# Kernel optimization log

Measured on AMD Instinct MI355X. Metric: run time of the kernel, lower is better.

## Reference

```python
import jax, jax.numpy as jnp
import numpy as np
from jax import lax

EXP = 5      # exponent bits of the custom float format
MAN = 10     # mantissa bits
STRIDE = 1
PADDING = 1


def float_quantize(x, exp=EXP, man=MAN):
    """Round-to-nearest-even quantization to a custom (exp, man) float format,
    with exponent clamping to the subnormal range and saturation at max value.
    Uses a straight-through estimator so the op is differentiable."""
    emax = 2 ** (exp - 1) - 1
    emin = 1 - emax
    _, e = jnp.frexp(x)                      # x = m * 2^e, m in [0.5, 1)
    e = jnp.maximum(e - 1, emin)             # unbiased exponent, clamp to emin (subnormals)
    scale = jnp.exp2((e - man).astype(x.dtype))
    q = jnp.round(x / scale) * scale         # round half to even on the mantissa grid
    maxval = jnp.asarray((2.0 - 2.0 ** (-man)) * 2.0 ** emax, x.dtype)
    q = jnp.clip(q, -maxval, maxval)
    return x + lax.stop_gradient(q - x)      # straight-through


def quant_gemm(a, b):
    """a: [M, K], b: [K, N]. FMA-style GEMM where the product and the running
    accumulator are re-quantized to the (EXP, MAN) format at every k step,
    mimicking the custom low-precision accumulation loop."""
    M = a.shape[0]
    N = b.shape[1]

    def step(acc, ab):
        ak, bk = ab                          # ak: [M], bk: [N]
        prod = float_quantize(ak[:, None] * bk[None, :])
        return float_quantize(acc + prod), None

    acc0 = jnp.zeros((M, N), a.dtype)
    acc, _ = lax.scan(step, acc0, (a.T, b))
    return acc


def _unfold(x, kh, kw, stride, padding):
    """im2col matching torch.nn.functional.unfold: returns [B, OH*OW, C*kh*kw]."""
    B, C, H, W = x.shape
    oh = (H - kh + 2 * padding) // stride + 1
    ow = (W - kw + 2 * padding) // stride + 1
    xp = jnp.pad(x, ((0, 0), (0, 0), (padding, padding), (padding, padding)))
    cols = []
    for i in range(kh):
        for j in range(kw):
            cols.append(xp[:, :, i:i + (oh - 1) * stride + 1:stride,
                              j:j + (ow - 1) * stride + 1:stride])
    col = jnp.stack(cols, axis=2)            # [B, C, kh*kw, oh, ow]
    col = col.reshape(B, C * kh * kw, oh * ow)
    return col.transpose(0, 2, 1), oh, ow    # [B, M, K]


def setup_inputs() -> dict:
    key = jax.random.key(0)
    kx, kw_, kb = jax.random.split(key, 3)
    x = jax.random.normal(kx, (16, 32, 56, 56), dtype=jnp.float32)
    # kaiming-uniform-ish scale: fan_in = 32*3*3 = 288
    weight = jax.random.normal(kw_, (64, 32, 3, 3), dtype=jnp.float32) * (1.0 / np.sqrt(288.0))
    bias = jax.random.normal(kb, (64,), dtype=jnp.float32) * (1.0 / np.sqrt(288.0))
    return {"x": x, "weight": weight, "bias": bias}


def reference(x, weight, bias):
    B, C, H, W = x.shape
    N, Cg, kh, kw = weight.shape
    qw = float_quantize(weight)              # quantize weights
    qb = float_quantize(bias)                # quantize bias
    a, oh, ow = _unfold(x, kh, kw, STRIDE, PADDING)   # [B, M, K]
    K = C * kh * kw
    a2 = a.reshape(B * oh * ow, K)
    b2 = qw.reshape(N, K).T                  # [K, N]
    out = quant_gemm(a2, b2)                 # [B*M, N], low-precision accumulation
    out = out + qb[None, :]
    out = float_quantize(out)                # re-quantize output
    out = out.reshape(B, oh * ow, N).transpose(0, 2, 1)
    return out.reshape(B, N, oh, ow)
```

## Files before the change

### kernel.cpp

```cpp
#include <hip/hip_runtime.h>
#include <stdint.h>

typedef _Float16 f16x8 __attribute__((ext_vector_type(8)));
typedef float    f32x4 __attribute__((ext_vector_type(4)));

#define H 56
#define W 56
#define C_IN 32
#define N_OUT 64
#define PR 58
#define PCOLS 66
#define XB_BLOCKS (16 * PR)
#define NWF 9216
#define XPAD_BYTES ((size_t)16 * PR * PCOLS * C_IN * 2)

__device__ __forceinline__ float q16f(float v) { return (float)(_Float16)v; }

__global__ __launch_bounds__(256) void prep_kernel(
    const float* __restrict__ x, const float* __restrict__ weight,
    _Float16* __restrict__ xpad, uint32_t* __restrict__ wf)
{
    const int nb  = blockIdx.x;
    const int tid = threadIdx.x;
    if (nb < XB_BLOCKS) {
        __shared__ _Float16 sT[PCOLS * 34];
        for (int i = tid; i < PCOLS * 17; i += 256) ((uint32_t*)sT)[i] = 0u;
        __syncthreads();
        const int b = nb / PR, row = nb % PR, ih = row - 1;
        if ((unsigned)ih < (unsigned)H) {
            #pragma unroll
            for (int k = 0; k < 7; ++k) {
                int idx = k * 256 + tid;
                int c = idx / W, iw = idx - c * W;
                sT[(iw + 1) * 34 + c] = (_Float16)x[((b * C_IN + c) * H + ih) * W + iw];
            }
        }
        __syncthreads();
        uint32_t* dst = (uint32_t*)(xpad + ((size_t)b * PR + row) * PCOLS * C_IN);
        for (int i = tid; i < PCOLS * 16; i += 256) {
            int col = i >> 4, cd = i & 15;
            dst[i] = ((const uint32_t*)sT)[col * 17 + cd];
        }
    } else {
        int o = (nb - XB_BLOCKS) * 256 + tid;
        int t2   = o & 3;
        int lane = (o >> 2) & 63;
        int u    = o >> 8;
        int nt   = u & 3, ij = u >> 2;
        int n    = nt * 16 + (lane & 15);
        int c0   = (lane >> 4) * 8 + 2 * t2;
        _Float16 lo = (_Float16)weight[n * 288 + c0 * 9 + ij];
        _Float16 hi = (_Float16)weight[n * 288 + (c0 + 1) * 9 + ij];
        wf[o] = (uint32_t)__builtin_bit_cast(uint16_t, lo) |
                ((uint32_t)__builtin_bit_cast(uint16_t, hi) << 16);
    }
}

__global__ __launch_bounds__(256, 2) void conv_mfma(
    const _Float16* __restrict__ xpad,
    const f16x8*    __restrict__ wf,
    const float*    __restrict__ bias,
    float* __restrict__ out)
{
    const int tid  = threadIdx.x;
    const int b    = blockIdx.z;
    const int oh   = blockIdx.y * 4 + (tid >> 6);
    const int bx   = blockIdx.x;
    const int ow0  = bx * 24;
    const int lane = tid & 63;
    const int quad = lane >> 4;
    const int px   = lane & 15;

    const _Float16* xb0 = xpad + (((size_t)b * PR + oh) * PCOLS + ow0 + px) * C_IN + quad * 8;
    const _Float16* xb1 = xb0 + 16 * C_IN;

    f32x4 acc[2][4] = {{{0,0,0,0},{0,0,0,0},{0,0,0,0},{0,0,0,0}},
                       {{0,0,0,0},{0,0,0,0},{0,0,0,0},{0,0,0,0}}};

    #pragma unroll
    for (int ij = 0; ij < 9; ++ij) {
        const int i = ij / 3, jj = ij - 3 * i;
        const int sh = (i * PCOLS + jj) * C_IN;
        f16x8 xf0 = *(const f16x8*)(xb0 + sh);
        f16x8 xf1 = *(const f16x8*)(xb1 + sh);
        #pragma unroll
        for (int nt = 0; nt < 4; ++nt) {
            f16x8 wv = wf[(ij * 4 + nt) * 64 + lane];
            acc[0][nt] = __builtin_amdgcn_mfma_f32_16x16x32_f16(wv, xf0, acc[0][nt], 0, 0, 0);
            acc[1][nt] = __builtin_amdgcn_mfma_f32_16x16x32_f16(wv, xf1, acc[1][nt], 0, 0, 0);
        }
    }

    #pragma unroll
    for (int xg = 0; xg < 2; ++xg) {
        const int ow = ow0 + 16 * xg + px;
        if (bx == 0 || ow >= 32) {
            #pragma unroll
            for (int nt = 0; nt < 4; ++nt) {
                #pragma unroll
                for (int reg = 0; reg < 4; ++reg) {
                    const int n = nt * 16 + quad * 4 + reg;
                    out[((size_t)(b * N_OUT + n) * H + oh) * W + ow] =
                        q16f(acc[xg][nt][reg] + q16f(bias[n]));
                }
            }
        }
    }
}

extern "C" void kernel_launch(void* const* d_in, const int* in_sizes, int n_in,
                              void* d_out, int out_size, void* d_ws, size_t ws_size,
                              hipStream_t stream) {
    const float* x      = (const float*)d_in[0];
    const float* weight = (const float*)d_in[1];
    const float* bias   = (const float*)d_in[2];
    float* out          = (float*)d_out;

    _Float16* xpad = (_Float16*)d_ws;
    uint32_t* wfp  = (uint32_t*)((char*)d_ws + XPAD_BYTES);

    prep_kernel<<<dim3(XB_BLOCKS + NWF / 256), dim3(256), 0, stream>>>(x, weight, xpad, wfp);
    conv_mfma<<<dim3(2, 14, 16), dim3(256), 0, stream>>>(xpad, (const f16x8*)wfp, bias, out);
}
```

Baseline: 71.83 us.

## Fuse input padding/transposition and weight packing into the conv kernel via LDS

Removes the separate prep kernel that wrote a padded fp16 NHWC copy of the input and packed weight fragments to global memory. Each conv block now loads its input halo tile directly from the fp32 NCHW input into shared memory, padded to 40 channels per pixel, and repacks all weights into shared memory itself. This drops one launch and the global round trip for the intermediate tensor. In exchange, every block redundantly repacks the full weight set and reads the input with a strided gather, and the shared-memory footprint is larger.

```diff
diff --git a/kernel.cpp b/kernel.cpp
--- a/kernel.cpp
+++ b/kernel.cpp
@@ -8,84 +8,77 @@
 #define W 56
 #define C_IN 32
 #define N_OUT 64
-#define PR 58
-#define PCOLS 66
-#define XB_BLOCKS (16 * PR)
-#define NWF 9216
-#define XPAD_BYTES ((size_t)16 * PR * PCOLS * C_IN * 2)
+#define CP 40
 
 __device__ __forceinline__ float q16f(float v) { return (float)(_Float16)v; }
 
-__global__ __launch_bounds__(256) void prep_kernel(
-    const float* __restrict__ x, const float* __restrict__ weight,
-    _Float16* __restrict__ xpad, uint32_t* __restrict__ wf)
+__global__ __launch_bounds__(256, 3) void conv_fused(
+    const float* __restrict__ x,
+    const float* __restrict__ weight,
+    const float* __restrict__ bias,
+    float* __restrict__ out)
 {
-    const int nb  = blockIdx.x;
+    __shared__ __align__(16) uint32_t sW[9216];
+    __shared__ __align__(16) _Float16 sX[6 * 34 * CP];
+
     const int tid = threadIdx.x;
-    if (nb < XB_BLOCKS) {
-        __shared__ _Float16 sT[PCOLS * 34];
-        for (int i = tid; i < PCOLS * 17; i += 256) ((uint32_t*)sT)[i] = 0u;
-        __syncthreads();
-        const int b = nb / PR, row = nb % PR, ih = row - 1;
-        if ((unsigned)ih < (unsigned)H) {
-            #pragma unroll
-            for (int k = 0; k < 7; ++k) {
-                int idx = k * 256 + tid;
-                int c = idx / W, iw = idx - c * W;
-                sT[(iw + 1) * 34 + c] = (_Float16)x[((b * C_IN + c) * H + ih) * W + iw];
-            }
-        }
-        __syncthreads();
-        uint32_t* dst = (uint32_t*)(xpad + ((size_t)b * PR + row) * PCOLS * C_IN);
-        for (int i = tid; i < PCOLS * 16; i += 256) {
-            int col = i >> 4, cd = i & 15;
-            dst[i] = ((const uint32_t*)sT)[col * 17 + cd];
-        }
-    } else {
-        int o = (nb - XB_BLOCKS) * 256 + tid;
+    const int b   = blockIdx.z;
+    const int oh0 = blockIdx.y * 4;
+    const int bx  = blockIdx.x;
+    const int ow0 = bx * 24;
+
+    #pragma unroll
+    for (int k = 0; k < 36; ++k) {
+        int o    = k * 256 + tid;
         int t2   = o & 3;
         int lane = (o >> 2) & 63;
         int u    = o >> 8;
         int nt   = u & 3, ij = u >> 2;
         int n    = nt * 16 + (lane & 15);
         int c0   = (lane >> 4) * 8 + 2 * t2;
-        _Float16 lo = (_Float16)weight[n * 288 + c0 * 9 + ij];
-        _Float16 hi = (_Float16)weight[n * 288 + (c0 + 1) * 9 + ij];
-        wf[o] = (uint32_t)__builtin_bit_cast(uint16_t, lo) |
+        const float* ws = weight + n * 288 + c0 * 9 + ij;
+        _Float16 lo = (_Float16)ws[0];
+        _Float16 hi = (_Float16)ws[9];
+        sW[o] = (uint32_t)__builtin_bit_cast(uint16_t, lo) |
                 ((uint32_t)__builtin_bit_cast(uint16_t, hi) << 16);
     }
-}
 
-__global__ __launch_bounds__(256, 2) void conv_mfma(
-    const _Float16* __restrict__ xpad,
-    const f16x8*    __restrict__ wf,
-    const float*    __restrict__ bias,
-    float* __restrict__ out)
-{
-    const int tid  = threadIdx.x;
-    const int b    = blockIdx.z;
-    const int oh   = blockIdx.y * 4 + (tid >> 6);
-    const int bx   = blockIdx.x;
-    const int ow0  = bx * 24;
+    #pragma unroll
+    for (int k = 0; k < 26; ++k) {
+        int f = k * 256 + tid;
+        if (f < 6528) {
+            int col = f % 34;
+            int u   = f / 34;
+            int r   = u % 6;
+            int c   = u / 6;
+            int ih = oh0 + r - 1, iw = ow0 + col - 1;
+            float v = 0.f;
+            if ((unsigned)ih < (unsigned)H && (unsigned)iw < (unsigned)W)
+                v = x[((b * C_IN + c) * H + ih) * W + iw];
+            sX[(r * 34 + col) * CP + c] = (_Float16)v;
+        }
+    }
+    __syncthreads();
+
+    const int wid  = tid >> 6;
     const int lane = tid & 63;
     const int quad = lane >> 4;
     const int px   = lane & 15;
-
-    const _Float16* xb0 = xpad + (((size_t)b * PR + oh) * PCOLS + ow0 + px) * C_IN + quad * 8;
-    const _Float16* xb1 = xb0 + 16 * C_IN;
+    const int oh   = oh0 + wid;
 
     f32x4 acc[2][4] = {{{0,0,0,0},{0,0,0,0},{0,0,0,0},{0,0,0,0}},
                        {{0,0,0,0},{0,0,0,0},{0,0,0,0},{0,0,0,0}}};
+    const f16x8* wfrag = (const f16x8*)sW;
 
     #pragma unroll
     for (int ij = 0; ij < 9; ++ij) {
         const int i = ij / 3, jj = ij - 3 * i;
-        const int sh = (i * PCOLS + jj) * C_IN;
-        f16x8 xf0 = *(const f16x8*)(xb0 + sh);
-        f16x8 xf1 = *(const f16x8*)(xb1 + sh);
+        const _Float16* xb = &sX[((wid + i) * 34 + px + jj) * CP + quad * 8];
+        f16x8 xf0 = *(const f16x8*)xb;
+        f16x8 xf1 = *(const f16x8*)(xb + 16 * CP);
         #pragma unroll
         for (int nt = 0; nt < 4; ++nt) {
-            f16x8 wv = wf[(ij * 4 + nt) * 64 + lane];
+            f16x8 wv = wfrag[(ij * 4 + nt) * 64 + lane];
             acc[0][nt] = __builtin_amdgcn_mfma_f32_16x16x32_f16(wv, xf0, acc[0][nt], 0, 0, 0);
             acc[1][nt] = __builtin_amdgcn_mfma_f32_16x16x32_f16(wv, xf1, acc[1][nt], 0, 0, 0);
         }
@@ -116,9 +109,5 @@
     const float* bias   = (const float*)d_in[2];
     float* out          = (float*)d_out;
 
-    _Float16* xpad = (_Float16*)d_ws;
-    uint32_t* wfp  = (uint32_t*)((char*)d_ws + XPAD_BYTES);
-
-    prep_kernel<<<dim3(XB_BLOCKS + NWF / 256), dim3(256), 0, stream>>>(x, weight, xpad, wfp);
-    conv_mfma<<<dim3(2, 14, 16), dim3(256), 0, stream>>>(xpad, (const f16x8*)wfp, bias, out);
+    conv_fused<<<dim3(2, 14, 16), dim3(256), 0, stream>>>(x, weight, bias, out);
 }
```

Result: slower. 76.53 us (+6.5%).

## Fuse prep and conv into one cooperative kernel with a grid sync

Applied to the files above, without the earlier changes.

Merges the padding/transpose prep kernel and the MFMA convolution into a single cooperatively launched kernel of 512 blocks, with a grid-wide sync between the two phases. This removes one kernel launch and its inter-kernel gap. The prep phase now uses a grid-stride loop that reads strided fp32 pairs directly instead of an LDS transpose, and the padded width shrinks from 66 to 58 columns. The risks are poorly coalesced global reads in the prep loop, the cost of the grid barrier, and a grid capped at 512 blocks for the compute phase.

```diff
diff --git a/kernel.cpp b/kernel.cpp
--- a/kernel.cpp
+++ b/kernel.cpp
@@ -1,5 +1,8 @@
 #include <hip/hip_runtime.h>
+#include <hip/hip_cooperative_groups.h>
 #include <stdint.h>
+
+namespace cg = cooperative_groups;
 
 typedef _Float16 f16x8 __attribute__((ext_vector_type(8)));
 typedef float    f32x4 __attribute__((ext_vector_type(4)));
@@ -9,67 +12,72 @@
 #define C_IN 32
 #define N_OUT 64
 #define PR 58
-#define PCOLS 66
-#define XB_BLOCKS (16 * PR)
+#define PCOLS 58
+#define NXT (16 * PR * PCOLS * 16)
 #define NWF 9216
-#define XPAD_BYTES ((size_t)16 * PR * PCOLS * C_IN * 2)
+#define NBLK 512
+#define NTHR (NBLK * 256)
 
 __device__ __forceinline__ float q16f(float v) { return (float)(_Float16)v; }
 
-__global__ __launch_bounds__(256) void prep_kernel(
-    const float* __restrict__ x, const float* __restrict__ weight,
-    _Float16* __restrict__ xpad, uint32_t* __restrict__ wf)
+__global__ __launch_bounds__(256, 2) void fused_kernel(
+    const float* __restrict__ x,
+    const float* __restrict__ weight,
+    const float* __restrict__ bias,
+    float* __restrict__ out,
+    uint32_t* __restrict__ xp,
+    uint32_t* __restrict__ wf)
 {
-    const int nb  = blockIdx.x;
     const int tid = threadIdx.x;
-    if (nb < XB_BLOCKS) {
-        __shared__ _Float16 sT[PCOLS * 34];
-        for (int i = tid; i < PCOLS * 17; i += 256) ((uint32_t*)sT)[i] = 0u;
-        __syncthreads();
-        const int b = nb / PR, row = nb % PR, ih = row - 1;
-        if ((unsigned)ih < (unsigned)H) {
-            #pragma unroll
-            for (int k = 0; k < 7; ++k) {
-                int idx = k * 256 + tid;
-                int c = idx / W, iw = idx - c * W;
-                sT[(iw + 1) * 34 + c] = (_Float16)x[((b * C_IN + c) * H + ih) * W + iw];
-            }
+    const int gid = blockIdx.x * 256 + tid;
+
+    for (int f = gid; f < NXT; f += NTHR) {
+        int cd  = f & 15;
+        int t   = f >> 4;
+        int col = t % PCOLS;
+        int t2  = t / PCOLS;
+        int row = t2 % PR;
+        int b   = t2 / PR;
+        int ih  = row - 1, iw = col - 1;
+        uint32_t dw = 0u;
+        if ((unsigned)ih < (unsigned)H && (unsigned)iw < (unsigned)W) {
+            const float* src = x + ((size_t)(b * C_IN + 2 * cd) * H + ih) * W + iw;
+            _Float16 lo = (_Float16)src[0];
+            _Float16 hi = (_Float16)src[H * W];
+            dw = (uint32_t)__builtin_bit_cast(uint16_t, lo) |
+                 ((uint32_t)__builtin_bit_cast(uint16_t, hi) << 16);
         }
-        __syncthreads();
-        uint32_t* dst = (uint32_t*)(xpad + ((size_t)b * PR + row) * PCOLS * C_IN);
-        for (int i = tid; i < PCOLS * 16; i += 256) {
-            int col = i >> 4, cd = i & 15;
-            dst[i] = ((const uint32_t*)sT)[col * 17 + cd];
-        }
-    } else {
-        int o = (nb - XB_BLOCKS) * 256 + tid;
-        int t2   = o & 3;
+        xp[f] = dw;
+    }
+
+    for (int o = gid; o < NWF; o += NTHR) {
+        int t2v  = o & 3;
         int lane = (o >> 2) & 63;
         int u    = o >> 8;
         int nt   = u & 3, ij = u >> 2;
         int n    = nt * 16 + (lane & 15);
-        int c0   = (lane >> 4) * 8 + 2 * t2;
+        int c0   = (lane >> 4) * 8 + 2 * t2v;
         _Float16 lo = (_Float16)weight[n * 288 + c0 * 9 + ij];
         _Float16 hi = (_Float16)weight[n * 288 + (c0 + 1) * 9 + ij];
         wf[o] = (uint32_t)__builtin_bit_cast(uint16_t, lo) |
                 ((uint32_t)__builtin_bit_cast(uint16_t, hi) << 16);
     }
-}
 
-__global__ __launch_bounds__(256, 2) void conv_mfma(
-    const _Float16* __restrict__ xpad,
-    const f16x8*    __restrict__ wf,
-    const float*    __restrict__ bias,
-    float* __restrict__ out)
-{
-    const int tid  = threadIdx.x;
-    const int b    = blockIdx.z;
-    const int oh   = blockIdx.y * 4 + (tid >> 6);
-    const int bx   = blockIdx.x;
-    const int ow0  = bx * 24;
+    cg::this_grid().sync();
+
+    const int wave = blockIdx.x * 4 + (tid >> 6);
+    if (wave >= 1792) return;
+    const int b    = wave / 112;
+    const int rem  = wave - b * 112;
+    const int owt  = rem / 56;
+    const int oh   = rem - owt * 56;
+    const int ow0  = owt * 24;
     const int lane = tid & 63;
     const int quad = lane >> 4;
     const int px   = lane & 15;
+
+    const _Float16* xpad = (const _Float16*)xp;
+    const f16x8*    wfv  = (const f16x8*)wf;
 
     const _Float16* xb0 = xpad + (((size_t)b * PR + oh) * PCOLS + ow0 + px) * C_IN + quad * 8;
     const _Float16* xb1 = xb0 + 16 * C_IN;
@@ -85,7 +93,7 @@
         f16x8 xf1 = *(const f16x8*)(xb1 + sh);
         #pragma unroll
         for (int nt = 0; nt < 4; ++nt) {
-            f16x8 wv = wf[(ij * 4 + nt) * 64 + lane];
+            f16x8 wv = wfv[(ij * 4 + nt) * 64 + lane];
             acc[0][nt] = __builtin_amdgcn_mfma_f32_16x16x32_f16(wv, xf0, acc[0][nt], 0, 0, 0);
             acc[1][nt] = __builtin_amdgcn_mfma_f32_16x16x32_f16(wv, xf1, acc[1][nt], 0, 0, 0);
         }
@@ -94,7 +102,7 @@
     #pragma unroll
     for (int xg = 0; xg < 2; ++xg) {
         const int ow = ow0 + 16 * xg + px;
-        if (bx == 0 || ow >= 32) {
+        if (owt == 0 || ow >= 32) {
             #pragma unroll
             for (int nt = 0; nt < 4; ++nt) {
                 #pragma unroll
@@ -116,9 +124,11 @@
     const float* bias   = (const float*)d_in[2];
     float* out          = (float*)d_out;
 
-    _Float16* xpad = (_Float16*)d_ws;
-    uint32_t* wfp  = (uint32_t*)((char*)d_ws + XPAD_BYTES);
+    uint32_t* xp = (uint32_t*)d_ws;
+    uint32_t* wf = (uint32_t*)((char*)d_ws + (size_t)NXT * 4);
 
-    prep_kernel<<<dim3(XB_BLOCKS + NWF / 256), dim3(256), 0, stream>>>(x, weight, xpad, wfp);
-    conv_mfma<<<dim3(2, 14, 16), dim3(256), 0, stream>>>(xpad, (const f16x8*)wfp, bias, out);
+    void* args[] = { (void*)&x, (void*)&weight, (void*)&bias,
+                     (void*)&out, (void*)&xp, (void*)&wf };
+    hipLaunchCooperativeKernel((const void*)fused_kernel, dim3(NBLK), dim3(256),
+                               args, 0, stream);
 }
```

Result: slower. 129.8 us (+80.8%).
